# Optimization experiments

Measured on AMD Instinct MI355X. Metric: run time of the kernel, lower is better.

## Reference

```python
import jax, jax.numpy as jnp
import numpy as np
from jax import lax

NEG = -1e30  # log-space 'zero' (avoid -inf for numerical safety)
EPS = 1e-7   # keras.backend.epsilon(), added before log in ctc_batch_cost


def _ctc_loss(y_pred, y_true):
    """CTC negative log-likelihood, full input/label lengths, blank = C-1.

    y_pred: [B, T, C] probabilities (post-softmax, as keras ctc_batch_cost expects)
    y_true: [B, L] int labels in [0, C-2]
    returns [B, 1] loss per example (matches keras ctc_batch_cost output shape)
    """
    B, T, C = y_pred.shape
    L = y_true.shape[1]
    S = 2 * L + 1
    blank = C - 1

    logp = jnp.log(y_pred + EPS)  # [B, T, C]

    # Extended label sequence: blank, l1, blank, l2, ..., lL, blank
    ext = jnp.full((B, S), blank, dtype=y_true.dtype)
    ext = ext.at[:, 1::2].set(y_true)  # [B, S]

    # s-2 skip transition allowed iff ext[s] != blank and ext[s] != ext[s-2]
    allow = jnp.concatenate(
        [jnp.zeros((B, 2), dtype=bool),
         (ext[:, 2:] != blank) & (ext[:, 2:] != ext[:, :-2])], axis=1)  # [B, S]

    # Gather log-probs of extended labels per time step: [T, B, S]
    logp_t = jnp.transpose(logp, (1, 0, 2))  # [T, B, C]
    idx = jnp.broadcast_to(ext[None, :, :], (T, B, S))
    lp_ext = jnp.take_along_axis(logp_t, idx, axis=2)  # [T, B, S]

    # alpha init at t=0: only s=0 (blank) and s=1 (first label) reachable
    alpha0 = jnp.full((B, S), NEG, dtype=logp.dtype)
    alpha0 = alpha0.at[:, 0].set(lp_ext[0, :, 0])
    alpha0 = alpha0.at[:, 1].set(lp_ext[0, :, 1])

    neg1 = jnp.full((B, 1), NEG, dtype=logp.dtype)
    neg2 = jnp.full((B, 2), NEG, dtype=logp.dtype)

    def step(alpha, lp):
        a1 = jnp.concatenate([neg1, alpha[:, :-1]], axis=1)
        a2 = jnp.concatenate([neg2, alpha[:, :-2]], axis=1)
        a = jnp.logaddexp(alpha, a1)
        a = jnp.logaddexp(a, jnp.where(allow, a2, NEG))
        return a + lp, None

    alphaT, _ = lax.scan(step, alpha0, lp_ext[1:])  # sequential over T-1 steps

    loss = -jnp.logaddexp(alphaT[:, S - 1], alphaT[:, S - 2])  # [B]
    return loss[:, None]


def setup_inputs() -> dict:
    key = jax.random.key(0)
    k1, k2 = jax.random.split(key)
    B, T, C, L = 512, 512, 128, 64
    logits = jax.random.normal(k1, (B, T, C), dtype=jnp.float32)
    y_pred = jax.nn.softmax(logits, axis=-1)  # ctc_batch_cost expects probabilities
    y_true = jax.random.randint(k2, (B, L), 0, C - 1)  # labels in [0, C-2]; blank=C-1
    return {"y_true": y_true, "y_pred": y_pred}


def reference(y_true, y_pred):
    return _ctc_loss(y_pred, y_true)
```

## Files before the change

kernel.cpp:

```cpp
#include <hip/hip_runtime.h>
#include <hip/hip_bf16.h>


typedef unsigned int u32;
typedef unsigned long long u64;

constexpr int B = 512, T = 512, C = 128, L = 64;
constexpr int BLANK = C - 1;
constexpr int NCHUNK = T / 8;
constexpr float EPS = 1e-7f;
constexpr float NEG = -1e30f;
constexpr float LN2 = 0.69314718055994530942f;

__device__ __forceinline__ u32 rne16(u32 b) {
    return (b + 0x7FFFu + ((b >> 16) & 1u)) >> 16;
}

__global__ __launch_bounds__(256)
void gather_kernel(const int* __restrict__ y_true,
                   const float* __restrict__ y_pred,
                   uint4* __restrict__ G2a,
                   uint4* __restrict__ G2b) {
    const int b    = blockIdx.x >> 1;
    const int half = blockIdx.x & 1;
    const int wave = threadIdx.x >> 6;
    const int lane = threadIdx.x & 63;

    const int lab  = y_true[b * L + lane];
    const int perm = (lab >> 1) << 2;
    const bool sel_hi = (lab & 1);

    const float2* __restrict__ base =
        (const float2*)(y_pred + (size_t)b * T * C) + lane;
    const int c0 = half * 32 + wave * 8;

    float2 buf[2][8];
#pragma unroll
    for (int j = 0; j < 8; ++j) buf[0][j] = base[(c0 * 8 + j) * 64];

#pragma unroll
    for (int i = 0; i < 8; ++i) {
        const int c = c0 + i;
        if (i + 1 < 8) {
#pragma unroll
            for (int j = 0; j < 8; ++j)
                buf[(i + 1) & 1][j] = base[((c + 1) * 8 + j) * 64];
        }
        const float2* row = buf[i & 1];

        u32 gl[8], gb[8];
#pragma unroll
        for (int j = 0; j < 8; ++j) {
            const int vx = __builtin_amdgcn_ds_bpermute(perm, __float_as_int(row[j].x));
            const int vy = __builtin_amdgcn_ds_bpermute(perm, __float_as_int(row[j].y));
            const float v = __int_as_float(sel_hi ? vy : vx) + EPS;
            gl[j] = __float_as_uint(v);
            gb[j] = __float_as_uint(__shfl(row[j].y, 63) + EPS);
        }
        u32 wl[4], wb[4];
#pragma unroll
        for (int q = 0; q < 4; ++q) {
            wl[q] = rne16(gl[2 * q]) | (rne16(gl[2 * q + 1]) << 16);
            wb[q] = rne16(gb[2 * q]) | (rne16(gb[2 * q + 1]) << 16);
        }
        G2a[(((size_t)b * NCHUNK + c) << 6) + lane] = make_uint4(wl[0], wl[1], wl[2], wl[3]);
        if (lane == 0)
            G2b[(size_t)b * NCHUNK + c] = make_uint4(wb[0], wb[1], wb[2], wb[3]);
    }
}

__device__ __forceinline__ double dpp64_shr1(double x) {
    union { double d; u32 u[2]; } in, out;
    in.d = x;
    out.u[0] = (u32)__builtin_amdgcn_update_dpp(0, (int)in.u[0], 0x138, 0xF, 0xF, false);
    out.u[1] = (u32)__builtin_amdgcn_update_dpp(0, (int)in.u[1], 0x138, 0xF, 0xF, false);
    return out.d;
}
template <int CTRL>
__device__ __forceinline__ u32 dpp_maxu_step(u32 m) {
    u32 t = (u32)__builtin_amdgcn_update_dpp(0, (int)m, CTRL, 0xF, 0xF, false);
    return m > t ? m : t;
}
__device__ __forceinline__ double exp2_exact(int e) {
    union { double d; u64 u; } s; s.u = (u64)(1023 + e) << 52; return s.d;
}

struct Bank { uint4 own[4]; uint4 blk[4]; };

__global__ __launch_bounds__(64, 1)
void scan_kernel(const int* __restrict__ y_true,
                 const uint4* __restrict__ G2a,
                 const uint4* __restrict__ G2b,
                 float* __restrict__ out) {
    const int b = blockIdx.x;
    const int l = threadIdx.x;

    const int lab = y_true[b * L + l];
    const int lab_prev = __shfl_up(lab, 1);
    const bool allow1 = (l >= 1) && (lab != lab_prev);

    const uint4* __restrict__ ownB = G2a + (((size_t)b * NCHUNK) << 6) + l;
    const uint4* __restrict__ blkB = G2b + (size_t)b * NCHUNK;

    auto load_bank = [&](Bank& bk, int c0) {
#pragma unroll
        for (int c = 0; c < 4; ++c) {
            bk.own[c] = ownB[(size_t)(c0 + c) << 6];
            bk.blk[c] = blkB[c0 + c];
        }
    };

    double d0 = (l == 0) ? 1.0 : 0.0;
    double d1 = 0.0;
    double d2 = 0.0;
    int Ce = 0;

    auto consume_bank = [&](const Bank& bk) {
#pragma unroll
        for (int c = 0; c < 4; ++c) {
            const u32* ow = (const u32*)&bk.own[c];
            const u32* bw = (const u32*)&bk.blk[c];
#pragma unroll
            for (int j = 0; j < 8; ++j) {
                const u32 wo = ow[j >> 1], wb = bw[j >> 1];
                const float fl = __uint_as_float((j & 1) ? (wo & 0xFFFF0000u) : (wo << 16));
                const float fb = __uint_as_float((j & 1) ? (wb & 0xFFFF0000u) : (wb << 16));
                const double Pl = (double)fl, Pb = (double)fb;
                const double p0  = dpp64_shr1(d1);
                const double sel = allow1 ? p0 : 0.0;
                const double nd0 = (d0 + p0) * Pb;
                const double nd2 = (d2 + d1) * Pb;
                const double nd1 = (d1 + (d0 + sel)) * Pl;
                d0 = nd0; d1 = nd1; d2 = nd2;
            }
        }
    };

    auto renorm = [&]() {
        u32 h0 = (u32)__double2hiint(d0);
        u32 h1 = (u32)__double2hiint(d1);
        u32 m = h0 > h1 ? h0 : h1;
        m = dpp_maxu_step<0x111>(m);
        m = dpp_maxu_step<0x112>(m);
        m = dpp_maxu_step<0x114>(m);
        m = dpp_maxu_step<0x118>(m);
        m = dpp_maxu_step<0x142>(m);
        m = dpp_maxu_step<0x143>(m);
        const u32 M = (u32)__builtin_amdgcn_readlane((int)m, 63);
        const int e = (int)((M >> 20) & 0x7FFu) - 1023;
        const double s = exp2_exact(-e);
        d0 *= s; d1 *= s; d2 *= s;
        Ce += e;
    };

    Bank A, Bk;
    load_bank(A, 0);
    load_bank(Bk, 4);

#pragma unroll 1
    for (int k = 0; k < 16; k += 2) {
        consume_bank(A);
        if (k + 2 < 16) load_bank(A, (k + 2) * 4);
        renorm();
        consume_bank(Bk);
        if (k + 3 < 16) load_bank(Bk, (k + 3) * 4);
        renorm();
    }

    if (l == 63) {
        const double sum = d1 + d2;
        const int ee = ((__double2hiint(sum) >> 20) & 0x7FF) - 1023;
        const float mant = (float)(sum * exp2_exact(-ee));
        out[b] = -((float)(Ce + ee) + __log2f(mant)) * LN2;
    }
}

__device__ __forceinline__ float lae2(float x, float y) {
    float m = fmaxf(x, y);
    float d = fminf(x, y) - m;
    return m + __logf(1.0f + __expf(d));
}
__device__ __forceinline__ float lae3(float x, float y, float z) {
    float m = fmaxf(fmaxf(x, y), z);
    float e = __expf(x - m) + __expf(y - m) + __expf(z - m);
    return m + __logf(e);
}
__global__ __launch_bounds__(64)
void ctc_fallback(const int* __restrict__ y_true,
                  const float* __restrict__ y_pred,
                  float* __restrict__ out) {
    const int b = blockIdx.x;
    const int l = threadIdx.x;
    const float* __restrict__ pb = y_pred + (size_t)b * T * C;
    const int lab = y_true[b * L + l];
    const int lab_prev = __shfl_up(lab, 1);
    const bool allow1 = (l >= 1) && (lab != lab_prev);
    float a0, a1, a2;
    {
        float pbl = pb[BLANK];
        float pla = pb[lab];
        a0 = (l == 0) ? __logf(pbl + EPS) : NEG;
        a1 = (l == 0) ? __logf(pla + EPS) : NEG;
        a2 = NEG;
    }
    for (int t = 1; t < T; ++t) {
        const float lpb = __logf(pb[t * C + BLANK] + EPS);
        const float lpl = __logf(pb[t * C + lab] + EPS);
        float p0 = __shfl_up(a1, 1);
        if (l == 0) p0 = NEG;
        const float na0 = lae2(a0, p0) + lpb;
        const float na1 = lae3(a1, a0, allow1 ? p0 : NEG) + lpl;
        const float na2 = lae2(a2, a1) + lpb;
        a0 = na0; a1 = na1; a2 = na2;
    }
    if (l == 63) out[b] = -lae2(a2, a1);
}

extern "C" void kernel_launch(void* const* d_in, const int* in_sizes, int n_in,
                              void* d_out, int out_size, void* d_ws, size_t ws_size,
                              hipStream_t stream) {
    const int*   y_true = (const int*)d_in[0];
    const float* y_pred = (const float*)d_in[1];
    float*       out    = (float*)d_out;

    const size_t nA = (size_t)B * NCHUNK * 64;
    const size_t nB = (size_t)B * NCHUNK;
    const size_t need = (nA + nB) * sizeof(uint4);
    if (ws_size >= need) {
        uint4* G2a = (uint4*)d_ws;
        uint4* G2b = G2a + nA;
        gather_kernel<<<dim3(B * 2), dim3(256), 0, stream>>>(y_true, y_pred, G2a, G2b);
        scan_kernel<<<dim3(B), dim3(64), 0, stream>>>(y_true, G2a, G2b, out);
    } else {
        ctc_fallback<<<dim3(B), dim3(64), 0, stream>>>(y_true, y_pred, out);
    }
}
```

Before: 213.0 us.

## Fuse gather and scan into one kernel staging bf16 probs in LDS

Merges the gather kernel and the scan kernel into a single 512-thread block per batch element. Eight waves gather and pack the label and blank probabilities into shared memory, then one wave runs the recurrence reading from LDS instead of a global workspace. This removes a launch and the round trip of the intermediate buffer through global memory. The cost is that seven waves sit idle during the serial scan, and the 66KB LDS footprint limits how many blocks fit per CU. The workspace fallback kernel is also removed, and the d0+d1 sum is hoisted to reshape the recurrence slightly.

```diff
diff --git a/kernel.cpp b/kernel.cpp
--- a/kernel.cpp
+++ b/kernel.cpp
@@ -6,69 +6,13 @@
 typedef unsigned long long u64;
 
 constexpr int B = 512, T = 512, C = 128, L = 64;
-constexpr int BLANK = C - 1;
 constexpr int NCHUNK = T / 8;
 constexpr float EPS = 1e-7f;
-constexpr float NEG = -1e30f;
 constexpr float LN2 = 0.69314718055994530942f;
 
 __device__ __forceinline__ u32 rne16(u32 b) {
     return (b + 0x7FFFu + ((b >> 16) & 1u)) >> 16;
 }
-
-__global__ __launch_bounds__(256)
-void gather_kernel(const int* __restrict__ y_true,
-                   const float* __restrict__ y_pred,
-                   uint4* __restrict__ G2a,
-                   uint4* __restrict__ G2b) {
-    const int b    = blockIdx.x >> 1;
-    const int half = blockIdx.x & 1;
-    const int wave = threadIdx.x >> 6;
-    const int lane = threadIdx.x & 63;
-
-    const int lab  = y_true[b * L + lane];
-    const int perm = (lab >> 1) << 2;
-    const bool sel_hi = (lab & 1);
-
-    const float2* __restrict__ base =
-        (const float2*)(y_pred + (size_t)b * T * C) + lane;
-    const int c0 = half * 32 + wave * 8;
-
-    float2 buf[2][8];
-#pragma unroll
-    for (int j = 0; j < 8; ++j) buf[0][j] = base[(c0 * 8 + j) * 64];
-
-#pragma unroll
-    for (int i = 0; i < 8; ++i) {
-        const int c = c0 + i;
-        if (i + 1 < 8) {
-#pragma unroll
-            for (int j = 0; j < 8; ++j)
-                buf[(i + 1) & 1][j] = base[((c + 1) * 8 + j) * 64];
-        }
-        const float2* row = buf[i & 1];
-
-        u32 gl[8], gb[8];
-#pragma unroll
-        for (int j = 0; j < 8; ++j) {
-            const int vx = __builtin_amdgcn_ds_bpermute(perm, __float_as_int(row[j].x));
-            const int vy = __builtin_amdgcn_ds_bpermute(perm, __float_as_int(row[j].y));
-            const float v = __int_as_float(sel_hi ? vy : vx) + EPS;
-            gl[j] = __float_as_uint(v);
-            gb[j] = __float_as_uint(__shfl(row[j].y, 63) + EPS);
-        }
-        u32 wl[4], wb[4];
-#pragma unroll
-        for (int q = 0; q < 4; ++q) {
-            wl[q] = rne16(gl[2 * q]) | (rne16(gl[2 * q + 1]) << 16);
-            wb[q] = rne16(gb[2 * q]) | (rne16(gb[2 * q + 1]) << 16);
-        }
-        G2a[(((size_t)b * NCHUNK + c) << 6) + lane] = make_uint4(wl[0], wl[1], wl[2], wl[3]);
-        if (lane == 0)
-            G2b[(size_t)b * NCHUNK + c] = make_uint4(wb[0], wb[1], wb[2], wb[3]);
-    }
-}
-
 __device__ __forceinline__ double dpp64_shr1(double x) {
     union { double d; u32 u[2]; } in, out;
     in.d = x;
@@ -87,30 +31,73 @@
 
 struct Bank { uint4 own[4]; uint4 blk[4]; };
 
-__global__ __launch_bounds__(64, 1)
-void scan_kernel(const int* __restrict__ y_true,
-                 const uint4* __restrict__ G2a,
-                 const uint4* __restrict__ G2b,
-                 float* __restrict__ out) {
-    const int b = blockIdx.x;
-    const int l = threadIdx.x;
+__global__ __launch_bounds__(512, 4)
+void ctc_fused(const int* __restrict__ y_true,
+               const float* __restrict__ y_pred,
+               float* __restrict__ out) {
+    __shared__ uint4 sG[NCHUNK * 65];
 
-    const int lab = y_true[b * L + l];
+    const int b    = blockIdx.x;
+    const int wave = threadIdx.x >> 6;
+    const int lane = threadIdx.x & 63;
+
+    const int lab  = y_true[b * L + lane];
+    const int perm = (lab >> 1) << 2;
+    const bool sel_hi = (lab & 1);
+
+    {
+        const float2* __restrict__ base =
+            (const float2*)(y_pred + (size_t)b * T * C) + lane;
+        const int c0 = wave * 8;
+
+        float2 buf[2][8];
+#pragma unroll
+        for (int j = 0; j < 8; ++j) buf[0][j] = base[(c0 * 8 + j) * 64];
+
+#pragma unroll
+        for (int i = 0; i < 8; ++i) {
+            const int c = c0 + i;
+            if (i + 1 < 8) {
+#pragma unroll
+                for (int j = 0; j < 8; ++j)
+                    buf[(i + 1) & 1][j] = base[((c + 1) * 8 + j) * 64];
+            }
+            const float2* row = buf[i & 1];
+
+            u32 gl[8], gb[8];
+#pragma unroll
+            for (int j = 0; j < 8; ++j) {
+                const int vx = __builtin_amdgcn_ds_bpermute(perm, __float_as_int(row[j].x));
+                const int vy = __builtin_amdgcn_ds_bpermute(perm, __float_as_int(row[j].y));
+                gl[j] = __float_as_uint(__int_as_float(sel_hi ? vy : vx) + EPS);
+                gb[j] = __float_as_uint(__shfl(row[j].y, 63) + EPS);
+            }
+            u32 wl[4], wb[4];
+#pragma unroll
+            for (int q = 0; q < 4; ++q) {
+                wl[q] = rne16(gl[2 * q]) | (rne16(gl[2 * q + 1]) << 16);
+                wb[q] = rne16(gb[2 * q]) | (rne16(gb[2 * q + 1]) << 16);
+            }
+            sG[c * 65 + lane] = make_uint4(wl[0], wl[1], wl[2], wl[3]);
+            if (lane == 0)
+                sG[c * 65 + 64] = make_uint4(wb[0], wb[1], wb[2], wb[3]);
+        }
+    }
+    __syncthreads();
+    if (threadIdx.x >= 64) return;
+
     const int lab_prev = __shfl_up(lab, 1);
-    const bool allow1 = (l >= 1) && (lab != lab_prev);
-
-    const uint4* __restrict__ ownB = G2a + (((size_t)b * NCHUNK) << 6) + l;
-    const uint4* __restrict__ blkB = G2b + (size_t)b * NCHUNK;
+    const bool allow1 = (lane >= 1) && (lab != lab_prev);
 
     auto load_bank = [&](Bank& bk, int c0) {
 #pragma unroll
         for (int c = 0; c < 4; ++c) {
-            bk.own[c] = ownB[(size_t)(c0 + c) << 6];
-            bk.blk[c] = blkB[c0 + c];
+            bk.own[c] = sG[(c0 + c) * 65 + lane];
+            bk.blk[c] = sG[(c0 + c) * 65 + 64];
         }
     };
 
-    double d0 = (l == 0) ? 1.0 : 0.0;
+    double d0 = (lane == 0) ? 1.0 : 0.0;
     double d1 = 0.0;
     double d2 = 0.0;
     int Ce = 0;
@@ -127,10 +114,11 @@
                 const float fb = __uint_as_float((j & 1) ? (wb & 0xFFFF0000u) : (wb << 16));
                 const double Pl = (double)fl, Pb = (double)fb;
                 const double p0  = dpp64_shr1(d1);
+                const double s01 = d0 + d1;
                 const double sel = allow1 ? p0 : 0.0;
                 const double nd0 = (d0 + p0) * Pb;
                 const double nd2 = (d2 + d1) * Pb;
-                const double nd1 = (d1 + (d0 + sel)) * Pl;
+                const double nd1 = (s01 + sel) * Pl;
                 d0 = nd0; d1 = nd1; d2 = nd2;
             }
         }
@@ -167,53 +155,12 @@
         renorm();
     }
 
-    if (l == 63) {
+    if (lane == 63) {
         const double sum = d1 + d2;
         const int ee = ((__double2hiint(sum) >> 20) & 0x7FF) - 1023;
         const float mant = (float)(sum * exp2_exact(-ee));
         out[b] = -((float)(Ce + ee) + __log2f(mant)) * LN2;
     }
-}
-
-__device__ __forceinline__ float lae2(float x, float y) {
-    float m = fmaxf(x, y);
-    float d = fminf(x, y) - m;
-    return m + __logf(1.0f + __expf(d));
-}
-__device__ __forceinline__ float lae3(float x, float y, float z) {
-    float m = fmaxf(fmaxf(x, y), z);
-    float e = __expf(x - m) + __expf(y - m) + __expf(z - m);
-    return m + __logf(e);
-}
-__global__ __launch_bounds__(64)
-void ctc_fallback(const int* __restrict__ y_true,
-                  const float* __restrict__ y_pred,
-                  float* __restrict__ out) {
-    const int b = blockIdx.x;
-    const int l = threadIdx.x;
-    const float* __restrict__ pb = y_pred + (size_t)b * T * C;
-    const int lab = y_true[b * L + l];
-    const int lab_prev = __shfl_up(lab, 1);
-    const bool allow1 = (l >= 1) && (lab != lab_prev);
-    float a0, a1, a2;
-    {
-        float pbl = pb[BLANK];
-        float pla = pb[lab];
-        a0 = (l == 0) ? __logf(pbl + EPS) : NEG;
-        a1 = (l == 0) ? __logf(pla + EPS) : NEG;
-        a2 = NEG;
-    }
-    for (int t = 1; t < T; ++t) {
-        const float lpb = __logf(pb[t * C + BLANK] + EPS);
-        const float lpl = __logf(pb[t * C + lab] + EPS);
-        float p0 = __shfl_up(a1, 1);
-        if (l == 0) p0 = NEG;
-        const float na0 = lae2(a0, p0) + lpb;
-        const float na1 = lae3(a1, a0, allow1 ? p0 : NEG) + lpl;
-        const float na2 = lae2(a2, a1) + lpb;
-        a0 = na0; a1 = na1; a2 = na2;
-    }
-    if (l == 63) out[b] = -lae2(a2, a1);
 }
 
 extern "C" void kernel_launch(void* const* d_in, const int* in_sizes, int n_in,
@@ -222,16 +169,5 @@
     const int*   y_true = (const int*)d_in[0];
     const float* y_pred = (const float*)d_in[1];
     float*       out    = (float*)d_out;
-
-    const size_t nA = (size_t)B * NCHUNK * 64;
-    const size_t nB = (size_t)B * NCHUNK;
-    const size_t need = (nA + nB) * sizeof(uint4);
-    if (ws_size >= need) {
-        uint4* G2a = (uint4*)d_ws;
-        uint4* G2b = G2a + nA;
-        gather_kernel<<<dim3(B * 2), dim3(256), 0, stream>>>(y_true, y_pred, G2a, G2b);
-        scan_kernel<<<dim3(B), dim3(64), 0, stream>>>(y_true, G2a, G2b, out);
-    } else {
-        ctc_fallback<<<dim3(B), dim3(64), 0, stream>>>(y_true, y_pred, out);
-    }
+    ctc_fused<<<dim3(B), dim3(512), 0, stream>>>(y_true, y_pred, out);
 }
```

Result: slower. 312.1 us (+46.5%).
